# Kernel tuning notes

Measured on AMD Instinct MI355X. Metric: run time of the kernel, lower is better.

The kernel has to match this reference:

```python
import jax, jax.numpy as jnp
import numpy as np

B, N, C = 128, 8732, 21  # batch, SSD priors, VOC classes (incl. background)
EPS = 1e-7


def setup_inputs() -> dict:
    key = jax.random.key(0)
    k1, k2, k3 = jax.random.split(key, 3)
    return {
        "lam": jnp.float32(0.7),
        "conf": jax.random.uniform(k1, (B, N, C), dtype=jnp.float32),
        "conf_shuffle": jax.random.uniform(k2, (B, N, C), dtype=jnp.float32),
        "conf_interpolation": jax.random.uniform(k3, (B, N, C), dtype=jnp.float32),
    }


def reference(lam, conf, conf_shuffle, conf_interpolation):
    half = conf.shape[0] // 2
    # swap the two halves of the shuffled batch
    conf_temp = jnp.concatenate([conf_shuffle[half:], conf_shuffle[:half]], axis=0)

    # foreground mask: max class score beats background score, on both sides
    left_mask = jnp.max(conf[..., 1:], axis=-1) > conf[..., 0]
    right_mask = jnp.max(conf_temp[..., 1:], axis=-1) > conf_temp[..., 0]
    mask = (left_mask & right_mask).astype(conf.dtype)  # [B, N]

    mixed = lam * conf + (1.0 - lam) * conf_temp + EPS
    inter = conf_interpolation + EPS

    sg = jax.lax.stop_gradient
    # KLDivLoss(log_input, target) = target * (log(target) - log_input), summed over classes
    inter_t = sg(inter)
    kl_a = jnp.sum(inter_t * (jnp.log(inter_t) - jnp.log(mixed)), axis=-1)  # [B, N]
    mixed_t = sg(mixed)
    kl_b = jnp.sum(mixed_t * (jnp.log(mixed_t) - jnp.log(inter)), axis=-1)  # [B, N]

    cnt = jnp.sum(mask)
    # masked mean over selected (b, n) samples; 0 if mask empty
    loss = jnp.sum((kl_a + kl_b) * mask) / jnp.maximum(cnt, 1.0)
    return jnp.where(cnt > 0, loss / 2.0, jnp.float32(0.0))
```

## Files before the change

kernel.cpp:

```cpp
#include <hip/hip_runtime.h>


#define EPS 1e-7f

constexpr int B = 128;
constexpr int N = 8732;
constexpr int C = 21;
constexpr int ROWS = B * N;
constexpr int CHUNK_ROWS = 64;
constexpr int CHUNK_ELEMS = CHUNK_ROWS * C;
constexpr int CHUNKS_PER_WAVE = 8;
constexpr int GRID = ROWS / (CHUNK_ROWS * CHUNKS_PER_WAVE);
constexpr int HALF_ELEMS = (B / 2) * N * C;

__global__ __launch_bounds__(64) void isd_main_kernel(
    const float* __restrict__ lam_p,
    const float* __restrict__ conf,
    const float* __restrict__ csh,
    const float* __restrict__ cin,
    double* __restrict__ partials)
{
    __shared__ float s_conf[CHUNK_ELEMS];
    __shared__ float s_csh [CHUNK_ELEMS];
    __shared__ float s_cin [CHUNK_ELEMS];

    const int lane = threadIdx.x;
    const float lam = lam_p[0];
    const float oml = 1.0f - lam;

    float sum = 0.0f;
    float cnt = 0.0f;

    const int chunk0 = blockIdx.x * CHUNKS_PER_WAVE;

    for (int ci = 0; ci < CHUNKS_PER_WAVE; ++ci) {
        const int base = (chunk0 + ci) * CHUNK_ELEMS;

        float rc[C], rs[C], ri[C];
        #pragma unroll
        for (int k = 0; k < C; ++k) {
            const int e = base + k * 64 + lane;
            rc[k] = conf[e];
            ri[k] = cin[e];
            const int e2 = (e < HALF_ELEMS) ? (e + HALF_ELEMS) : (e - HALF_ELEMS);
            rs[k] = csh[e2];
        }
        #pragma unroll
        for (int k = 0; k < C; ++k) {
            s_conf[k * 64 + lane] = rc[k];
            s_csh [k * 64 + lane] = rs[k];
            s_cin [k * 64 + lane] = ri[k];
        }

        const float* pc = s_conf + lane * C;
        const float* pt = s_csh  + lane * C;
        const float* pi = s_cin  + lane * C;

        float c0 = 0.0f, t0 = 0.0f;
        float cmax = -1e30f, tmax = -1e30f;
        float kl = 0.0f;

        #pragma unroll
        for (int c = 0; c < C; ++c) {
            const float cv = pc[c];
            const float tv = pt[c];
            const float iv = pi[c] + EPS;
            const float mv = fmaf(lam, cv, oml * tv) + EPS;
            kl += (iv - mv) * (__logf(iv) - __logf(mv));
            if (c == 0) { c0 = cv; t0 = tv; }
            else        { cmax = fmaxf(cmax, cv); tmax = fmaxf(tmax, tv); }
        }

        const float msk = ((cmax > c0) && (tmax > t0)) ? 1.0f : 0.0f;
        sum += kl * msk;
        cnt += msk;
    }

    #pragma unroll
    for (int off = 32; off > 0; off >>= 1) {
        sum += __shfl_down(sum, off, 64);
        cnt += __shfl_down(cnt, off, 64);
    }

    if (lane == 0) {
        partials[2 * blockIdx.x + 0] = (double)sum;
        partials[2 * blockIdx.x + 1] = (double)cnt;
    }
}

__global__ __launch_bounds__(256) void isd_final_kernel(
    const double* __restrict__ partials,
    float* __restrict__ out)
{
    double s = 0.0, c = 0.0;
    for (int i = threadIdx.x; i < GRID; i += 256) {
        s += partials[2 * i + 0];
        c += partials[2 * i + 1];
    }
    #pragma unroll
    for (int off = 32; off > 0; off >>= 1) {
        s += __shfl_down(s, off, 64);
        c += __shfl_down(c, off, 64);
    }
    __shared__ double ss[4], sc[4];
    const int wave = threadIdx.x >> 6;
    const int lane = threadIdx.x & 63;
    if (lane == 0) { ss[wave] = s; sc[wave] = c; }
    __syncthreads();
    if (threadIdx.x == 0) {
        const double S  = ss[0] + ss[1] + ss[2] + ss[3];
        const double Cc = sc[0] + sc[1] + sc[2] + sc[3];
        out[0] = (Cc > 0.0) ? (float)(S / fmax(Cc, 1.0) * 0.5) : 0.0f;
    }
}

extern "C" void kernel_launch(void* const* d_in, const int* in_sizes, int n_in,
                              void* d_out, int out_size, void* d_ws, size_t ws_size,
                              hipStream_t stream) {
    const float* lam  = (const float*)d_in[0];
    const float* conf = (const float*)d_in[1];
    const float* csh  = (const float*)d_in[2];
    const float* cin  = (const float*)d_in[3];
    float* out = (float*)d_out;
    double* partials = (double*)d_ws;

    isd_main_kernel<<<GRID, 64, 0, stream>>>(lam, conf, csh, cin, partials);
    isd_final_kernel<<<1, 256, 0, stream>>>(partials, out);
}
```

Before: 283.5 us.

## Double-buffer chunk loads in registers and halve chunks per wave

```diff
diff --git a/kernel.cpp b/kernel.cpp
--- a/kernel.cpp
+++ b/kernel.cpp
@@ -9,9 +9,26 @@
 constexpr int ROWS = B * N;
 constexpr int CHUNK_ROWS = 64;
 constexpr int CHUNK_ELEMS = CHUNK_ROWS * C;
-constexpr int CHUNKS_PER_WAVE = 8;
-constexpr int GRID = ROWS / (CHUNK_ROWS * CHUNKS_PER_WAVE);
+constexpr int CPW = 4;
+constexpr int GRID = ROWS / (CHUNK_ROWS * CPW);
 constexpr int HALF_ELEMS = (B / 2) * N * C;
+
+__device__ __forceinline__ void stage_load(
+    const float* __restrict__ conf,
+    const float* __restrict__ csh,
+    const float* __restrict__ cin,
+    int base, int lane,
+    float* rc, float* rs, float* ri)
+{
+    #pragma unroll
+    for (int k = 0; k < C; ++k) {
+        const int e = base + k * 64 + lane;
+        rc[k] = conf[e];
+        ri[k] = cin[e];
+        const int e2 = (e < HALF_ELEMS) ? (e + HALF_ELEMS) : (e - HALF_ELEMS);
+        rs[k] = csh[e2];
+    }
+}
 
 __global__ __launch_bounds__(64) void isd_main_kernel(
     const float* __restrict__ lam_p,
@@ -31,25 +48,23 @@
     float sum = 0.0f;
     float cnt = 0.0f;
 
-    const int chunk0 = blockIdx.x * CHUNKS_PER_WAVE;
+    const int chunk0 = blockIdx.x * CPW;
 
-    for (int ci = 0; ci < CHUNKS_PER_WAVE; ++ci) {
-        const int base = (chunk0 + ci) * CHUNK_ELEMS;
+    float A0[C], A1[C], A2[C];
+    float B0[C], B1[C], B2[C];
 
-        float rc[C], rs[C], ri[C];
+    stage_load(conf, csh, cin, chunk0 * CHUNK_ELEMS, lane, A0, A1, A2);
+
+    #pragma unroll
+    for (int ci = 0; ci < CPW; ++ci) {
+        if (ci + 1 < CPW)
+            stage_load(conf, csh, cin, (chunk0 + ci + 1) * CHUNK_ELEMS, lane, B0, B1, B2);
+
         #pragma unroll
         for (int k = 0; k < C; ++k) {
-            const int e = base + k * 64 + lane;
-            rc[k] = conf[e];
-            ri[k] = cin[e];
-            const int e2 = (e < HALF_ELEMS) ? (e + HALF_ELEMS) : (e - HALF_ELEMS);
-            rs[k] = csh[e2];
-        }
-        #pragma unroll
-        for (int k = 0; k < C; ++k) {
-            s_conf[k * 64 + lane] = rc[k];
-            s_csh [k * 64 + lane] = rs[k];
-            s_cin [k * 64 + lane] = ri[k];
+            s_conf[k * 64 + lane] = A0[k];
+            s_csh [k * 64 + lane] = A1[k];
+            s_cin [k * 64 + lane] = A2[k];
         }
 
         const float* pc = s_conf + lane * C;
@@ -74,6 +89,11 @@
         const float msk = ((cmax > c0) && (tmax > t0)) ? 1.0f : 0.0f;
         sum += kl * msk;
         cnt += msk;
+
+        if (ci + 1 < CPW) {
+            #pragma unroll
+            for (int k = 0; k < C; ++k) { A0[k] = B0[k]; A1[k] = B1[k]; A2[k] = B2[k]; }
+        }
     }
 
     #pragma unroll
```

Result: no change. 281.6 us (-0.7%).
